# Optimization experiments

Measured on AMD Instinct MI355X. Metric: run time of the kernel, lower is better.

Reference implementation:

```python
import jax, jax.numpy as jnp
import numpy as np

E, IN, H1, H2, H3, A, B = 20, 512, 1024, 512, 256, 32, 4096


def setup_inputs() -> dict:
    key = jax.random.key(0)
    ks = jax.random.split(key, 10)

    def w(k, shape, fan_in):
        return jax.random.normal(k, shape, dtype=jnp.float32) / np.sqrt(fan_in)

    return {
        "obs": jax.random.normal(ks[0], (B, IN), dtype=jnp.float32),
        # stacked expert MLP params [E, ...]
        "eW1": w(ks[1], (E, IN, H1), IN), "eb1": jnp.zeros((E, H1), jnp.float32),
        "eW2": w(ks[2], (E, H1, H2), H1), "eb2": jnp.zeros((E, H2), jnp.float32),
        "eW3": w(ks[3], (E, H2, H3), H2), "eb3": jnp.zeros((E, H3), jnp.float32),
        "eW4": w(ks[4], (E, H3, A), H3), "eb4": jnp.zeros((E, A), jnp.float32),
        # gate MLP params
        "gW1": w(ks[5], (IN, H1), IN), "gb1": jnp.zeros((H1,), jnp.float32),
        "gW2": w(ks[6], (H1, H2), H1), "gb2": jnp.zeros((H2,), jnp.float32),
        "gW3": w(ks[7], (H2, H3), H2), "gb3": jnp.zeros((H3,), jnp.float32),
        "gW4": w(ks[8], (H3, E), H3), "gb4": jnp.zeros((E,), jnp.float32),
    }


def _experts(obs, eW1, eb1, eW2, eb2, eW3, eb3, eW4, eb4):
    # batched over experts: [B, E, h]
    h = jax.nn.elu(jnp.einsum('bi,eih->beh', obs, eW1) + eb1[None])
    h = jax.nn.elu(jnp.einsum('beh,ehk->bek', h, eW2) + eb2[None])
    h = jax.nn.elu(jnp.einsum('bek,ekm->bem', h, eW3) + eb3[None])
    return jnp.einsum('bem,ema->bea', h, eW4) + eb4[None]  # [B, E, A]


def _gate(obs, gW1, gb1, gW2, gb2, gW3, gb3, gW4, gb4):
    h = jax.nn.elu(obs @ gW1 + gb1)
    h = jax.nn.elu(h @ gW2 + gb2)
    h = jax.nn.elu(h @ gW3 + gb3)
    return jax.nn.softmax(h @ gW4 + gb4, axis=-1)  # [B, E]


def reference(obs, eW1, eb1, eW2, eb2, eW3, eb3, eW4, eb4,
              gW1, gb1, gW2, gb2, gW3, gb3, gW4, gb4):
    weights = _gate(obs, gW1, gb1, gW2, gb2, gW3, gb3, gW4, gb4)       # [B, E]
    actions = _experts(obs, eW1, eb1, eW2, eb2, eW3, eb3, eW4, eb4)    # [B, E, A]
    # bmm(weights[:,None,:], actions).squeeze(1)
    return jnp.einsum('be,bea->ba', weights, actions)                   # [B, A]
```

## Files before the change

kernel.cpp:

```cpp
#include <hip/hip_runtime.h>

#define B_SZ 4096
#define E_EXP 20
#define NE 21

typedef unsigned short u16;
typedef __bf16 bf16x8 __attribute__((ext_vector_type(8)));
typedef u16 u16x8 __attribute__((ext_vector_type(8)));
typedef u16 u16x4 __attribute__((ext_vector_type(4)));
typedef float floatx4 __attribute__((ext_vector_type(4)));

static __device__ __forceinline__ u16 f2bf(float f) {
  unsigned u = __builtin_bit_cast(unsigned, f);
  u += 0x7fffu + ((u >> 16) & 1u);
  return (u16)(u >> 16);
}

static __device__ __forceinline__ float elu1(float v) {
  return v > 0.f ? v : (__expf(v) - 1.f);
}

static __device__ __forceinline__ bf16x8 ld_bf8(const u16* p) {
  u16x8 v = *reinterpret_cast<const u16x8*>(p);
  return __builtin_bit_cast(bf16x8, v);
}

static __device__ __forceinline__ void gld_lds16(const u16* g, u16* l) {
  __builtin_amdgcn_global_load_lds(
      (const __attribute__((address_space(1))) unsigned int*)g,
      (__attribute__((address_space(3))) unsigned int*)l, 16, 0, 0);
}


__global__ void prep_small_kernel(
    const float* __restrict__ obs, u16* __restrict__ obs_bf,
    const float* __restrict__ eb1, const float* __restrict__ gb1,
    const float* __restrict__ eb2, const float* __restrict__ gb2,
    const float* __restrict__ eb3, const float* __restrict__ gb3,
    float* __restrict__ b1, float* __restrict__ b2, float* __restrict__ b3) {
  int bid = blockIdx.x;
  if (bid < 2048) {
    int i = (bid * 256 + threadIdx.x) * 4;
    float4 v = *reinterpret_cast<const float4*>(obs + i);
    u16x4 o;
    o.x = f2bf(v.x); o.y = f2bf(v.y); o.z = f2bf(v.z); o.w = f2bf(v.w);
    *reinterpret_cast<u16x4*>(obs_bf + i) = o;
  } else {
    int i = (bid - 2048) * 256 + threadIdx.x;
    const int S1 = NE * 1024, S2 = NE * 512, S3 = NE * 256;
    if (i < S1) {
      b1[i] = (i < E_EXP * 1024) ? eb1[i] : gb1[i - E_EXP * 1024];
    } else if (i < S1 + S2) {
      int j = i - S1;
      b2[j] = (j < E_EXP * 512) ? eb2[j] : gb2[j - E_EXP * 512];
    } else if (i < S1 + S2 + S3) {
      int j = i - S1 - S2;
      b3[j] = (j < E_EXP * 256) ? eb3[j] : gb3[j - E_EXP * 256];
    }
  }
}

#define TRANS_BLOCKS 6132

__global__ __launch_bounds__(256) void transpose_all_kernel(
    const float* __restrict__ eW1, const float* __restrict__ gW1,
    const float* __restrict__ eW2, const float* __restrict__ gW2,
    const float* __restrict__ eW3, const float* __restrict__ gW3,
    const float* __restrict__ eW4, const float* __restrict__ gW4,
    u16* __restrict__ W1t, u16* __restrict__ W2t, u16* __restrict__ W3t,
    u16* __restrict__ W4t, u16* __restrict__ gW4t) {
  int f = blockIdx.x;
  const float *srcE, *srcG;
  u16* dstBase;
  int rem, K, N, Nout, kxt, tpm, nm;
  if (f < 2688) {
    rem = f;        srcE = eW1; srcG = gW1; dstBase = W1t;
    K = 512;  N = 1024; Nout = 1024; kxt = 8;  tpm = 128; nm = 20;
  } else if (f < 5376) {
    rem = f - 2688; srcE = eW2; srcG = gW2; dstBase = W2t;
    K = 1024; N = 512;  Nout = 512;  kxt = 16; tpm = 128; nm = 20;
  } else if (f < 6048) {
    rem = f - 5376; srcE = eW3; srcG = gW3; dstBase = W3t;
    K = 512;  N = 256;  Nout = 256;  kxt = 8;  tpm = 32;  nm = 20;
  } else if (f < 6128) {
    rem = f - 6048; srcE = eW4; srcG = nullptr; dstBase = W4t;
    K = 256;  N = 32;   Nout = 32;   kxt = 4;  tpm = 4;   nm = 99;
  } else {
    rem = f - 6128; srcE = gW4; srcG = nullptr; dstBase = gW4t;
    K = 256;  N = 20;   Nout = 32;   kxt = 4;  tpm = 4;   nm = 99;
  }
  int mat = rem / tpm;
  int t = rem % tpm;
  const float* src = (mat < nm) ? (srcE + (long)mat * K * N) : srcG;
  u16* dst = dstBase + (long)mat * Nout * K;
  int kbase = (t % kxt) * 64;
  int nbase = (t / kxt) * 64;

  __shared__ float tl[64][65];
  int tid = threadIdx.x;
  int kk = tid >> 4;
  int n4 = (tid & 15) * 4;
#pragma unroll
  for (int p = 0; p < 4; ++p) {
    int k = kbase + p * 16 + kk;
    int n = nbase + n4;
    float4 v = make_float4(0.f, 0.f, 0.f, 0.f);
    if (n + 3 < N) {
      v = *reinterpret_cast<const float4*>(&src[(long)k * N + n]);
    } else {
      float* vp = &v.x;
      for (int j = 0; j < 4; ++j)
        if (n + j < N) vp[j] = src[(long)k * N + n + j];
    }
    tl[p * 16 + kk][n4 + 0] = v.x;
    tl[p * 16 + kk][n4 + 1] = v.y;
    tl[p * 16 + kk][n4 + 2] = v.z;
    tl[p * 16 + kk][n4 + 3] = v.w;
  }
  __syncthreads();

  int kk8 = (tid & 7) * 8;
#pragma unroll
  for (int p = 0; p < 2; ++p) {
    int ln = p * 32 + (tid >> 3);
    int n = nbase + ln;
    if (n < Nout) {
      u16x8 o;
#pragma unroll
      for (int j = 0; j < 8; ++j) o[j] = f2bf(tl[kk8 + j][ln]);
      *reinterpret_cast<u16x8*>(&dst[(long)n * K + kbase + kk8]) = o;
    }
  }
}


#define BM 128
#define BN 128

__global__ __launch_bounds__(256) void gemm_bias_elu_kernel(
    const u16* __restrict__ A_base, long a_estride,
    const u16* __restrict__ Wt_base, long w_estride,
    const float* __restrict__ bias_base, long b_estride,
    u16* __restrict__ C_base, long c_estride,
    int M, int N, int K, int ntn, int ntm) {
  int per = gridDim.x >> 3;
  int wid = (blockIdx.x & 7) * per + (blockIdx.x >> 3);
  int tpe = ntn * ntm;
  int e = wid / tpe;
  int rem = wid - e * tpe;
  int mt = rem / ntn;
  int nt = rem - mt * ntn;
  int m0 = mt * BM;
  int n0 = nt * BN;

  const u16* A = A_base + (long)e * a_estride;
  const u16* Wt = Wt_base + (long)e * w_estride;
  const float* bias = bias_base + (long)e * b_estride;
  u16* C = C_base + (long)e * c_estride;

  __shared__ u16 As[BM * 64];
  __shared__ u16 Bs[BN * 64];

  int tid = threadIdx.x;
  int lane = tid & 63;
  int w = tid >> 6;
  int wm = (w >> 1) * 64;
  int wn = (w & 1) * 64;
  int col = lane & 15;
  int quad = lane >> 4;

  floatx4 acc[4][4] = {};

  int srow = tid >> 3;
  int gchunk = (tid & 7) ^ (srow & 7);
  const u16* gA = &A[(long)(m0 + srow) * K + gchunk * 8];
  const u16* gB = &Wt[(long)(n0 + srow) * K + gchunk * 8];
  long rowK = (long)32 * K;

  int s0 = (quad ^ (col & 7)) * 8;
  int aRow = (wm + col) * 64;
  int bRow = (wn + col) * 64;

  for (int k0 = 0; k0 < K; k0 += 64) {
    __syncthreads();
    gld_lds16(gA + k0,            &As[(size_t)tid * 8]);
    gld_lds16(gA + rowK + k0,     &As[2048 + (size_t)tid * 8]);
    gld_lds16(gA + 2 * rowK + k0, &As[4096 + (size_t)tid * 8]);
    gld_lds16(gA + 3 * rowK + k0, &As[6144 + (size_t)tid * 8]);
    gld_lds16(gB + k0,            &Bs[(size_t)tid * 8]);
    gld_lds16(gB + rowK + k0,     &Bs[2048 + (size_t)tid * 8]);
    gld_lds16(gB + 2 * rowK + k0, &Bs[4096 + (size_t)tid * 8]);
    gld_lds16(gB + 3 * rowK + k0, &Bs[6144 + (size_t)tid * 8]);
    __syncthreads();

#pragma unroll
    for (int kk = 0; kk < 2; ++kk) {
      int s = s0 ^ (kk * 32);
      bf16x8 xf[4], wf[4];
#pragma unroll
      for (int t = 0; t < 4; ++t) {
        xf[t] = __builtin_bit_cast(bf16x8,
            *reinterpret_cast<u16x8*>(&As[aRow + t * 1024 + s]));
        wf[t] = __builtin_bit_cast(bf16x8,
            *reinterpret_cast<u16x8*>(&Bs[bRow + t * 1024 + s]));
      }
#pragma unroll
      for (int i = 0; i < 4; ++i)
#pragma unroll
        for (int j = 0; j < 4; ++j)
          acc[i][j] = __builtin_amdgcn_mfma_f32_16x16x32_bf16(
              wf[j], xf[i], acc[i][j], 0, 0, 0);
    }
  }

#pragma unroll
  for (int j = 0; j < 4; ++j) {
    int nn = n0 + wn + j * 16 + quad * 4;
    float4 b4 = *reinterpret_cast<const float4*>(&bias[nn]);
#pragma unroll
    for (int i = 0; i < 4; ++i) {
      int m = m0 + wm + i * 16 + col;
      u16x4 o;
      o.x = f2bf(elu1(acc[i][j][0] + b4.x));
      o.y = f2bf(elu1(acc[i][j][1] + b4.y));
      o.z = f2bf(elu1(acc[i][j][2] + b4.z));
      o.w = f2bf(elu1(acc[i][j][3] + b4.w));
      *reinterpret_cast<u16x4*>(&C[(long)m * N + nn]) = o;
    }
  }
}

__global__ __launch_bounds__(256) void final_combine_kernel(
    const u16* __restrict__ h3, const u16* __restrict__ W4t,
    const u16* __restrict__ gW4t, const float* __restrict__ eb4,
    const float* __restrict__ gb4, float* __restrict__ out) {
  const int H3 = 256;
  int tid = threadIdx.x;
  int lane = tid & 63;
  int w = tid >> 6;
  int col = lane & 15;
  int quad = lane >> 4;
  int r0 = blockIdx.x * 16;

  floatx4 g0 = {}, g1 = {};
  const u16* h3g = h3 + (long)E_EXP * B_SZ * H3;
#pragma unroll
  for (int k0 = 0; k0 < 256; k0 += 32) {
    bf16x8 a = ld_bf8(&h3g[(long)(r0 + col) * H3 + k0 + quad * 8]);
    bf16x8 b0 = ld_bf8(&gW4t[(long)col * H3 + k0 + quad * 8]);
    bf16x8 b1 = ld_bf8(&gW4t[(long)(16 + col) * H3 + k0 + quad * 8]);
    g0 = __builtin_amdgcn_mfma_f32_16x16x32_bf16(a, b0, g0, 0, 0, 0);
    g1 = __builtin_amdgcn_mfma_f32_16x16x32_bf16(a, b1, g1, 0, 0, 0);
  }

  float w0[4], w1[4];
  float gbc0 = gb4[col];
  float gbc1 = (col < 4) ? gb4[16 + col] : 0.f;
#pragma unroll
  for (int r = 0; r < 4; ++r) {
    float v0 = g0[r] + gbc0;
    float v1 = (col < 4) ? (g1[r] + gbc1) : -1e30f;
    float m = fmaxf(v0, v1);
#pragma unroll
    for (int s = 1; s < 16; s <<= 1) m = fmaxf(m, __shfl_xor(m, s, 64));
    float e0 = __expf(v0 - m);
    float e1 = (col < 4) ? __expf(v1 - m) : 0.f;
    float ssum = e0 + e1;
#pragma unroll
    for (int s = 1; s < 16; s <<= 1) ssum += __shfl_xor(ssum, s, 64);
    w0[r] = e0 / ssum;
    w1[r] = e1 / ssum;
  }

  floatx4 o0 = {}, o1 = {};
  for (int e = w; e < E_EXP; e += 4) {
    floatx4 a0 = {}, a1 = {};
    const u16* he = h3 + (long)e * B_SZ * H3;
    const u16* we = W4t + (long)e * 32 * H3;
#pragma unroll
    for (int k0 = 0; k0 < 256; k0 += 32) {
      bf16x8 a = ld_bf8(&he[(long)(r0 + col) * H3 + k0 + quad * 8]);
      bf16x8 b0 = ld_bf8(&we[(long)col * H3 + k0 + quad * 8]);
      bf16x8 b1 = ld_bf8(&we[(long)(16 + col) * H3 + k0 + quad * 8]);
      a0 = __builtin_amdgcn_mfma_f32_16x16x32_bf16(a, b0, a0, 0, 0, 0);
      a1 = __builtin_amdgcn_mfma_f32_16x16x32_bf16(a, b1, a1, 0, 0, 0);
    }
    float be0 = eb4[e * 32 + col];
    float be1 = eb4[e * 32 + 16 + col];
    int src = (lane & 48) + (e & 15);
#pragma unroll
    for (int r = 0; r < 4; ++r) {
      float wr = __shfl((e < 16) ? w0[r] : w1[r], src, 64);
      o0[r] += wr * (a0[r] + be0);
      o1[r] += wr * (a1[r] + be1);
    }
  }

  __shared__ float red[3][64][8];
  if (w > 0) {
#pragma unroll
    for (int r = 0; r < 4; ++r) {
      red[w - 1][lane][r] = o0[r];
      red[w - 1][lane][4 + r] = o1[r];
    }
  }
  __syncthreads();
  if (w == 0) {
#pragma unroll
    for (int ww = 0; ww < 3; ++ww)
#pragma unroll
      for (int r = 0; r < 4; ++r) {
        o0[r] += red[ww][lane][r];
        o1[r] += red[ww][lane][4 + r];
      }
#pragma unroll
    for (int r = 0; r < 4; ++r) {
      int row = r0 + quad * 4 + r;
      out[(long)row * 32 + col] = o0[r];
      out[(long)row * 32 + 16 + col] = o1[r];
    }
  }
}


static inline size_t align256(size_t x) { return (x + 255) & ~(size_t)255; }

extern "C" void kernel_launch(void* const* d_in, const int* in_sizes, int n_in,
                              void* d_out, int out_size, void* d_ws,
                              size_t ws_size, hipStream_t stream) {
  const float* obs = (const float*)d_in[0];
  const float* eW1 = (const float*)d_in[1];
  const float* eb1 = (const float*)d_in[2];
  const float* eW2 = (const float*)d_in[3];
  const float* eb2 = (const float*)d_in[4];
  const float* eW3 = (const float*)d_in[5];
  const float* eb3 = (const float*)d_in[6];
  const float* eW4 = (const float*)d_in[7];
  const float* eb4 = (const float*)d_in[8];
  const float* gW1 = (const float*)d_in[9];
  const float* gb1 = (const float*)d_in[10];
  const float* gW2 = (const float*)d_in[11];
  const float* gb2 = (const float*)d_in[12];
  const float* gW3 = (const float*)d_in[13];
  const float* gb3 = (const float*)d_in[14];
  const float* gW4 = (const float*)d_in[15];
  const float* gb4 = (const float*)d_in[16];
  float* out = (float*)d_out;
  char* ws = (char*)d_ws;

  size_t off = 0;
  size_t OFF_OBS = off;  off = align256(off + (size_t)B_SZ * 512 * 2);
  size_t OFF_W1T = off;  off = align256(off + (size_t)NE * 1024 * 512 * 2);
  size_t OFF_W2T = off;  off = align256(off + (size_t)NE * 512 * 1024 * 2);
  size_t OFF_W3T = off;  off = align256(off + (size_t)NE * 256 * 512 * 2);
  size_t OFF_W4T = off;  off = align256(off + (size_t)E_EXP * 32 * 256 * 2);
  size_t OFF_GW4T = off; off = align256(off + (size_t)32 * 256 * 2);
  size_t OFF_B1 = off;   off = align256(off + (size_t)NE * 1024 * 4);
  size_t OFF_B2 = off;   off = align256(off + (size_t)NE * 512 * 4);
  size_t OFF_B3 = off;   off = align256(off + (size_t)NE * 256 * 4);
  size_t OFF_H3 = off;   off = align256(off + (size_t)NE * B_SZ * 256 * 2);

  int chunk = B_SZ;
  size_t OFF_H1 = off;
  while (chunk > 512) {
    size_t need = (size_t)NE * chunk * 1024 * 2 + (size_t)NE * chunk * 512 * 2;
    if (OFF_H1 + need <= ws_size) break;
    chunk >>= 1;
  }
  size_t OFF_H2 = align256(OFF_H1 + (size_t)NE * chunk * 1024 * 2);

  u16* obs_bf = (u16*)(ws + OFF_OBS);
  u16* W1t = (u16*)(ws + OFF_W1T);
  u16* W2t = (u16*)(ws + OFF_W2T);
  u16* W3t = (u16*)(ws + OFF_W3T);
  u16* W4t = (u16*)(ws + OFF_W4T);
  u16* gW4t = (u16*)(ws + OFF_GW4T);
  float* b1 = (float*)(ws + OFF_B1);
  float* b2 = (float*)(ws + OFF_B2);
  float* b3 = (float*)(ws + OFF_B3);
  u16* h3 = (u16*)(ws + OFF_H3);
  u16* h1 = (u16*)(ws + OFF_H1);
  u16* h2 = (u16*)(ws + OFF_H2);

  prep_small_kernel<<<2048 + (NE * 1792 + 255) / 256, 256, 0, stream>>>(
      obs, obs_bf, eb1, gb1, eb2, gb2, eb3, gb3, b1, b2, b3);
  transpose_all_kernel<<<TRANS_BLOCKS, 256, 0, stream>>>(
      eW1, gW1, eW2, gW2, eW3, gW3, eW4, gW4, W1t, W2t, W3t, W4t, gW4t);

  int ntm = chunk / BM;
  for (int bc = 0; bc < B_SZ; bc += chunk) {
    gemm_bias_elu_kernel<<<NE * 8 * ntm, 256, 0, stream>>>(
        obs_bf + (size_t)bc * 512, 0L,
        W1t, (long)1024 * 512,
        b1, 1024L,
        h1, (long)chunk * 1024, chunk, 1024, 512, 8, ntm);
    gemm_bias_elu_kernel<<<NE * 4 * ntm, 256, 0, stream>>>(
        h1, (long)chunk * 1024,
        W2t, (long)512 * 1024,
        b2, 512L,
        h2, (long)chunk * 512, chunk, 512, 1024, 4, ntm);
    gemm_bias_elu_kernel<<<NE * 2 * ntm, 256, 0, stream>>>(
        h2, (long)chunk * 512,
        W3t, (long)256 * 512,
        b3, 256L,
        h3 + (size_t)bc * 256, (long)B_SZ * 256, chunk, 256, 512, 2, ntm);
  }

  final_combine_kernel<<<B_SZ / 16, 256, 0, stream>>>(h3, W4t, gW4t, eb4, gb4,
                                                      out);
}
```

Before: 504.1 us.

## Double-buffer LDS tiles to overlap global loads with MFMA compute

Splits the shared-memory A and B tiles into two buffers. The next K-slice is issued into one buffer while MFMAs consume the other, which hides global-to-LDS load latency behind compute and removes one barrier per iteration. This doubles LDS use per block, which may reduce occupancy. The loop steps 128 at a time and always computes on the second buffer, so it assumes K is a multiple of 128.

After: 497.9 us. About the same (-1.2%).

```diff
diff --git a/kernel.cpp b/kernel.cpp
--- a/kernel.cpp
+++ b/kernel.cpp
@@ -158,8 +158,10 @@
   const float* bias = bias_base + (long)e * b_estride;
   u16* C = C_base + (long)e * c_estride;
 
-  __shared__ u16 As[BM * 64];
-  __shared__ u16 Bs[BN * 64];
+  __shared__ u16 As0[BM * 64];
+  __shared__ u16 As1[BM * 64];
+  __shared__ u16 Bs0[BN * 64];
+  __shared__ u16 Bs1[BN * 64];
 
   int tid = threadIdx.x;
   int lane = tid & 63;
@@ -181,37 +183,53 @@
   int aRow = (wm + col) * 64;
   int bRow = (wn + col) * 64;
 
-  for (int k0 = 0; k0 < K; k0 += 64) {
+#define STAGE(Asb, Bsb, k0)                                   \
+  do {                                                        \
+    gld_lds16(gA + (k0),            &Asb[(size_t)tid * 8]);   \
+    gld_lds16(gA + rowK + (k0),     &Asb[2048 + (size_t)tid * 8]); \
+    gld_lds16(gA + 2 * rowK + (k0), &Asb[4096 + (size_t)tid * 8]); \
+    gld_lds16(gA + 3 * rowK + (k0), &Asb[6144 + (size_t)tid * 8]); \
+    gld_lds16(gB + (k0),            &Bsb[(size_t)tid * 8]);   \
+    gld_lds16(gB + rowK + (k0),     &Bsb[2048 + (size_t)tid * 8]); \
+    gld_lds16(gB + 2 * rowK + (k0), &Bsb[4096 + (size_t)tid * 8]); \
+    gld_lds16(gB + 3 * rowK + (k0), &Bsb[6144 + (size_t)tid * 8]); \
+  } while (0)
+
+#define COMPUTE(Asb, Bsb)                                               \
+  do {                                                                  \
+    _Pragma("unroll")                                                   \
+    for (int kk = 0; kk < 2; ++kk) {                                    \
+      int s = s0 ^ (kk * 32);                                           \
+      bf16x8 xf[4], wf[4];                                              \
+      _Pragma("unroll")                                                 \
+      for (int t4 = 0; t4 < 4; ++t4) {                                  \
+        xf[t4] = __builtin_bit_cast(bf16x8,                             \
+            *reinterpret_cast<const u16x8*>(&Asb[aRow + t4 * 1024 + s])); \
+        wf[t4] = __builtin_bit_cast(bf16x8,                             \
+            *reinterpret_cast<const u16x8*>(&Bsb[bRow + t4 * 1024 + s])); \
+      }                                                                 \
+      _Pragma("unroll")                                                 \
+      for (int i = 0; i < 4; ++i)                                       \
+        _Pragma("unroll")                                               \
+        for (int j = 0; j < 4; ++j)                                     \
+          acc[i][j] = __builtin_amdgcn_mfma_f32_16x16x32_bf16(          \
+              wf[j], xf[i], acc[i][j], 0, 0, 0);                        \
+    }                                                                   \
+  } while (0)
+
+  STAGE(As0, Bs0, 0);
+  __syncthreads();
+
+  for (int k0 = 0; k0 < K; k0 += 128) {
+    if (k0 + 64 < K) STAGE(As1, Bs1, k0 + 64);
+    COMPUTE(As0, Bs0);
     __syncthreads();
-    gld_lds16(gA + k0,            &As[(size_t)tid * 8]);
-    gld_lds16(gA + rowK + k0,     &As[2048 + (size_t)tid * 8]);
-    gld_lds16(gA + 2 * rowK + k0, &As[4096 + (size_t)tid * 8]);
-    gld_lds16(gA + 3 * rowK + k0, &As[6144 + (size_t)tid * 8]);
-    gld_lds16(gB + k0,            &Bs[(size_t)tid * 8]);
-    gld_lds16(gB + rowK + k0,     &Bs[2048 + (size_t)tid * 8]);
-    gld_lds16(gB + 2 * rowK + k0, &Bs[4096 + (size_t)tid * 8]);
-    gld_lds16(gB + 3 * rowK + k0, &Bs[6144 + (size_t)tid * 8]);
+    if (k0 + 128 < K) STAGE(As0, Bs0, k0 + 128);
+    COMPUTE(As1, Bs1);
     __syncthreads();
-
-#pragma unroll
-    for (int kk = 0; kk < 2; ++kk) {
-      int s = s0 ^ (kk * 32);
-      bf16x8 xf[4], wf[4];
-#pragma unroll
-      for (int t = 0; t < 4; ++t) {
-        xf[t] = __builtin_bit_cast(bf16x8,
-            *reinterpret_cast<u16x8*>(&As[aRow + t * 1024 + s]));
-        wf[t] = __builtin_bit_cast(bf16x8,
-            *reinterpret_cast<u16x8*>(&Bs[bRow + t * 1024 + s]));
-      }
-#pragma unroll
-      for (int i = 0; i < 4; ++i)
-#pragma unroll
-        for (int j = 0; j < 4; ++j)
-          acc[i][j] = __builtin_amdgcn_mfma_f32_16x16x32_bf16(
-              wf[j], xf[i], acc[i][j], 0, 0, 0);
-    }
-  }
+  }
+#undef STAGE
+#undef COMPUTE
 
 #pragma unroll
   for (int j = 0; j < 4; ++j) {
```
